# Kernel tuning notes

Hardware: AMD Instinct MI355X
Metric: run time of the kernel (lower is better)

## Reference

```python
import jax, jax.numpy as jnp
import numpy as np

L2 = (0.01, 0.01)
L1_RATIO = 0.5
EPS = 1e-16


def soft_thresholding(x, t):
    return jnp.sign(x) * jnp.maximum(jnp.abs(x) - t, 0.0)


def update_u(x, u, v, l1, l2, eps=EPS):
    # x: [B,M,N], u: [B,M,R], v: [B,N,R]
    a = jnp.einsum('bmn,bnr->bmr', x, v)      # x @ v            [B,M,R]
    b = jnp.einsum('bnr,bns->brs', v, v)      # v.mT @ v         [B,R,R]
    R = u.shape[-1]

    def step(u_new, r):
        # Gauss-Seidel update of column r using the freshest u_new (sequential dependency)
        br = jnp.take(b, r, axis=-1)                        # b[..., :, r]   [B,R]
        brr = jnp.take(br, r, axis=-1)                      # b[..., r, r]   [B]
        # term2 = u_new[..., indices] @ b[..., indices, r] computed as full matvec minus the r-th term
        term2 = jnp.einsum('bmk,bk->bm', u_new, br) - jnp.take(u_new, r, axis=-1) * brr[:, None]
        num = soft_thresholding(jnp.take(a, r, axis=-1) - term2, l1)   # [B,M]
        den = brr[:, None] + l2                                        # [B,1]
        ur = (num + eps) / (den + eps)
        return u_new.at[..., r].set(ur), None

    u_new, _ = jax.lax.scan(step, u, jnp.arange(R))
    return u_new


def setup_inputs() -> dict:
    key = jax.random.key(0)
    k1, k2, k3 = jax.random.split(key, 3)
    B, M, N, R = 8, 2048, 2048, 32
    x = jax.random.normal(k1, (B, M, N), dtype=jnp.float32)
    u = jax.random.normal(k2, (B, M, R), dtype=jnp.float32)
    v = jax.random.normal(k3, (B, N, R), dtype=jnp.float32)
    return {"x": x, "u": u, "v": v}


def reference(x, u, v):
    M, N = x.shape[-2], x.shape[-1]
    l1_u = L2[0] * L1_RATIO * N
    l2_u = L2[0] * (1.0 - L1_RATIO) * N
    l1_v = L2[1] * L1_RATIO * M
    l2_v = L2[1] * (1.0 - L1_RATIO) * M
    u = update_u(x, u, v, l1_u, l2_u)                              # factor 0
    v = update_u(jnp.swapaxes(x, -1, -2), v, u, l1_v, l2_v)        # factor 1 (update_v)
    return (u, v)
```

## Files before the change

kernel.cpp:

```cpp
#include <hip/hip_runtime.h>
#include <hip/hip_bf16.h>

#define NB 8
#define MD 2048
#define RD 32
#define KSPLIT 4
#define KSL (2048 / KSPLIT)
#define VT_STRIDE 520
#define XT_STRIDE 40
#define ASL ((size_t)NB * 2048 * RD)

typedef float floatx4 __attribute__((ext_vector_type(4)));
typedef short shortx8 __attribute__((ext_vector_type(8)));

static __device__ __forceinline__ short f2b(float f) {
    __hip_bfloat16 h = __float2bfloat16(f);
    return (short)*reinterpret_cast<unsigned short*>(&h);
}

static __device__ __forceinline__ void bmat_part(const float* __restrict__ w,
                                                 float* __restrict__ bp,
                                                 int bz, int t, char* smem) {
    int batch = bz >> 5;
    int slice = bz & 31;
    float* ws = (float*)smem;
    const float* wb = w + ((size_t)batch * 2048 + slice * 64) * RD;
#pragma unroll
    for (int i = 0; i < 8; ++i) {
        int idx = t + i * 256;
        ws[(idx >> 5) * 36 + (idx & 31)] = wb[(idx >> 5) * RD + (idx & 31)];
    }
    __syncthreads();
    int ii = t >> 3;
    int jq = (t & 7) * 4;
    float a0 = 0.f, a1 = 0.f, a2 = 0.f, a3 = 0.f;
    for (int n = 0; n < 64; ++n) {
        float wi = ws[n * 36 + ii];
        float4 wj = *(const float4*)&ws[n * 36 + jq];
        a0 = fmaf(wi, wj.x, a0);
        a1 = fmaf(wi, wj.y, a1);
        a2 = fmaf(wi, wj.z, a2);
        a3 = fmaf(wi, wj.w, a3);
    }
    float4 r = {a0, a1, a2, a3};
    *(float4*)(bp + (((size_t)batch * 32 + slice) * RD + ii) * RD + jq) = r;
}

__global__ __launch_bounds__(256, 4) void fused1_kernel(const float* __restrict__ x,
                                                        const float* __restrict__ v,
                                                        float* __restrict__ ap,
                                                        float* __restrict__ bp) {
    __shared__ __align__(16) char smem[32 * VT_STRIDE * 2];
    int bz = blockIdx.x;
    int t = threadIdx.x;
    if (bz < NB * 32) {
        bmat_part(v, bp, bz, t, smem);
        return;
    }
    bz -= NB * 32;
    short* wT = (short*)smem;
    int ks = bz & (KSPLIT - 1);
    int mblk = (bz >> 2) & 31;
    int batch = bz >> 7;
    int lane = t & 63;
    int wave = t >> 6;

    const float* wb = v + ((size_t)batch * 2048 + ks * KSL) * RD;
#pragma unroll
    for (int i = 0; i < 16; ++i) {
        int idx = t + i * 256;
        int k = idx >> 3;
        int rq = (idx & 7) * 4;
        float4 f = *(const float4*)(wb + (size_t)k * RD + rq);
        wT[(rq + 0) * VT_STRIDE + k] = f2b(f.x);
        wT[(rq + 1) * VT_STRIDE + k] = f2b(f.y);
        wT[(rq + 2) * VT_STRIDE + k] = f2b(f.z);
        wT[(rq + 3) * VT_STRIDE + k] = f2b(f.w);
    }
    __syncthreads();

    int kq = (lane >> 4) * 8;
    const float* xrow =
        x + ((size_t)batch * MD + mblk * 64 + wave * 16 + (lane & 15)) * 2048 + ks * KSL + kq;
    int r0 = (lane & 15) * VT_STRIDE + kq;
    int r1 = ((lane & 15) + 16) * VT_STRIDE + kq;

    floatx4 acc0 = {0.f, 0.f, 0.f, 0.f}, acc1 = {0.f, 0.f, 0.f, 0.f};
    float4 fa = *(const float4*)(xrow);
    float4 fb = *(const float4*)(xrow + 4);
    for (int s = 0; s < KSL / 32; ++s) {
        float4 na = {0, 0, 0, 0}, nb = {0, 0, 0, 0};
        if (s + 1 < KSL / 32) {
            na = *(const float4*)(xrow + (s + 1) * 32);
            nb = *(const float4*)(xrow + (s + 1) * 32 + 4);
        }
        shortx8 af = {f2b(fa.x), f2b(fa.y), f2b(fa.z), f2b(fa.w),
                      f2b(fb.x), f2b(fb.y), f2b(fb.z), f2b(fb.w)};
        shortx8 b0 = *(const shortx8*)&wT[r0 + s * 32];
        shortx8 b1 = *(const shortx8*)&wT[r1 + s * 32];
        acc0 = __builtin_amdgcn_mfma_f32_16x16x32_bf16(af, b0, acc0, 0, 0, 0);
        acc1 = __builtin_amdgcn_mfma_f32_16x16x32_bf16(af, b1, acc1, 0, 0, 0);
        fa = na;
        fb = nb;
    }
    float* ab = ap + ks * ASL +
                ((size_t)batch * 2048 + mblk * 64 + wave * 16 + (lane >> 4) * 4) * RD +
                (lane & 15);
#pragma unroll
    for (int i = 0; i < 4; ++i) {
        ab[i * RD] = acc0[i];
        ab[i * RD + 16] = acc1[i];
    }
}

__global__ __launch_bounds__(256, 4) void fused2_kernel(const float* __restrict__ x,
                                                        const float* __restrict__ u,
                                                        float* __restrict__ ap,
                                                        float* __restrict__ bp) {
    __shared__ __align__(16) short smem[32 * VT_STRIDE + 4 * 16 * XT_STRIDE];
    int bz = blockIdx.x;
    int t = threadIdx.x;
    if (bz < NB * 32) {
        bmat_part(u, bp, bz, t, (char*)smem);
        return;
    }
    bz -= NB * 32;
    short* uT = smem;
    short* xT = smem + 32 * VT_STRIDE;
    int ks = bz & (KSPLIT - 1);
    int nblk = (bz >> 2) & 31;
    int batch = bz >> 7;
    int lane = t & 63;
    int wave = t >> 6;

    const float* ub = u + ((size_t)batch * 2048 + ks * KSL) * RD;
#pragma unroll
    for (int i = 0; i < 16; ++i) {
        int idx = t + i * 256;
        int k = idx >> 3;
        int rq = (idx & 7) * 4;
        float4 f = *(const float4*)(ub + (size_t)k * RD + rq);
        uT[(rq + 0) * VT_STRIDE + k] = f2b(f.x);
        uT[(rq + 1) * VT_STRIDE + k] = f2b(f.y);
        uT[(rq + 2) * VT_STRIDE + k] = f2b(f.z);
        uT[(rq + 3) * VT_STRIDE + k] = f2b(f.w);
    }
    __syncthreads();

    short* xTw = &xT[wave * 16 * XT_STRIDE];
    int mloc = lane & 31;
    int ng = (lane >> 5) * 8;
    int n0w = nblk * 64 + wave * 16;
    const float* xp = x + ((size_t)batch * 2048 + ks * KSL + mloc) * 2048 + n0w + ng;

    int nl = lane & 15;
    int kq = (lane >> 4) * 8;
    int rA = nl * XT_STRIDE + kq;
    int rB0 = nl * VT_STRIDE + kq;
    int rB1 = (nl + 16) * VT_STRIDE + kq;

    floatx4 acc0 = {0.f, 0.f, 0.f, 0.f}, acc1 = {0.f, 0.f, 0.f, 0.f};
    float4 fa = *(const float4*)xp;
    float4 fb = *(const float4*)(xp + 4);
    for (int s = 0; s < KSL / 32; ++s) {
        xTw[(ng + 0) * XT_STRIDE + mloc] = f2b(fa.x);
        xTw[(ng + 1) * XT_STRIDE + mloc] = f2b(fa.y);
        xTw[(ng + 2) * XT_STRIDE + mloc] = f2b(fa.z);
        xTw[(ng + 3) * XT_STRIDE + mloc] = f2b(fa.w);
        xTw[(ng + 4) * XT_STRIDE + mloc] = f2b(fb.x);
        xTw[(ng + 5) * XT_STRIDE + mloc] = f2b(fb.y);
        xTw[(ng + 6) * XT_STRIDE + mloc] = f2b(fb.z);
        xTw[(ng + 7) * XT_STRIDE + mloc] = f2b(fb.w);
        float4 na = {0, 0, 0, 0}, nb = {0, 0, 0, 0};
        if (s + 1 < KSL / 32) {
            na = *(const float4*)(xp + (size_t)(s + 1) * 32 * 2048);
            nb = *(const float4*)(xp + (size_t)(s + 1) * 32 * 2048 + 4);
        }
        shortx8 af = *(const shortx8*)&xTw[rA];
        shortx8 b0 = *(const shortx8*)&uT[rB0 + s * 32];
        shortx8 b1 = *(const shortx8*)&uT[rB1 + s * 32];
        acc0 = __builtin_amdgcn_mfma_f32_16x16x32_bf16(af, b0, acc0, 0, 0, 0);
        acc1 = __builtin_amdgcn_mfma_f32_16x16x32_bf16(af, b1, acc1, 0, 0, 0);
        fa = na;
        fb = nb;
    }
    float* ab = ap + ks * ASL +
                ((size_t)batch * 2048 + n0w + (lane >> 4) * 4) * RD + (lane & 15);
#pragma unroll
    for (int i = 0; i < 4; ++i) {
        ab[i * RD] = acc0[i];
        ab[i * RD + 16] = acc1[i];
    }
}

__global__ __launch_bounds__(256) void gs_kernel(const float* __restrict__ uin,
                                                 const float* __restrict__ ap,
                                                 const float* __restrict__ bp,
                                                 float* __restrict__ uout,
                                                 float l1, float l2) {
    int blk = blockIdx.x;
    int batch = blk >> 3;
    int m = (blk & 7) * 256 + threadIdx.x;
    __shared__ float bs[RD][RD];
    {
        const float4* bpp = (const float4*)(bp + (size_t)batch * 32 * RD * RD) + threadIdx.x;
        float4 bacc = {0.f, 0.f, 0.f, 0.f};
#pragma unroll
        for (int s = 0; s < 32; ++s) {
            float4 f = bpp[s * 256];
            bacc.x += f.x;
            bacc.y += f.y;
            bacc.z += f.z;
            bacc.w += f.w;
        }
        ((float4*)&bs[0][0])[threadIdx.x] = bacc;
    }
    __syncthreads();
    float uv[RD], av[RD];
    const float* up = uin + ((size_t)batch * 2048 + m) * RD;
    const float* app = ap + ((size_t)batch * 2048 + m) * RD;
#pragma unroll
    for (int q = 0; q < 8; ++q) {
        *(float4*)&uv[q * 4] = *(const float4*)&up[q * 4];
        float4 s0 = *(const float4*)(app + q * 4);
        float4 s1 = *(const float4*)(app + ASL + q * 4);
        float4 s2 = *(const float4*)(app + 2 * ASL + q * 4);
        float4 s3 = *(const float4*)(app + 3 * ASL + q * 4);
        float4 r;
        r.x = (s0.x + s1.x) + (s2.x + s3.x);
        r.y = (s0.y + s1.y) + (s2.y + s3.y);
        r.z = (s0.z + s1.z) + (s2.z + s3.z);
        r.w = (s0.w + s1.w) + (s2.w + s3.w);
        *(float4*)&av[q * 4] = r;
    }
#pragma unroll
    for (int r = 0; r < RD; ++r) {
        float brr = bs[r][r];
        float4 t2v = {0.f, 0.f, 0.f, 0.f};
#pragma unroll
        for (int q = 0; q < 8; ++q) {
            float4 bq = *(const float4*)&bs[r][q * 4];
            t2v.x = fmaf(uv[q * 4 + 0], bq.x, t2v.x);
            t2v.y = fmaf(uv[q * 4 + 1], bq.y, t2v.y);
            t2v.z = fmaf(uv[q * 4 + 2], bq.z, t2v.z);
            t2v.w = fmaf(uv[q * 4 + 3], bq.w, t2v.w);
        }
        float t2 = ((t2v.x + t2v.y) + (t2v.z + t2v.w)) - uv[r] * brr;
        float num = av[r] - t2;
        float mag = fmaxf(fabsf(num) - l1, 0.f);
        num = copysignf(mag, num);
        uv[r] = (num + 1e-16f) / (brr + l2 + 1e-16f);
    }
    float* op = uout + ((size_t)batch * 2048 + m) * RD;
#pragma unroll
    for (int q = 0; q < 8; ++q) *(float4*)&op[q * 4] = *(float4*)&uv[q * 4];
}

extern "C" void kernel_launch(void* const* d_in, const int* in_sizes, int n_in,
                              void* d_out, int out_size, void* d_ws, size_t ws_size,
                              hipStream_t stream) {
    const float* x = (const float*)d_in[0];
    const float* u = (const float*)d_in[1];
    const float* v = (const float*)d_in[2];
    float* out_u = (float*)d_out;
    float* out_v = out_u + (size_t)NB * MD * RD;
    float* ap = (float*)d_ws;
    float* bp = ap + KSPLIT * ASL;
    const float l1u = 10.24f, l2u = 10.24f;
    const float l1v = 10.24f, l2v = 10.24f;
    const int GRID = NB * 32 + NB * 32 * KSPLIT;

    fused1_kernel<<<GRID, 256, 0, stream>>>(x, v, ap, bp);
    gs_kernel<<<NB * 8, 256, 0, stream>>>(u, ap, bp, out_u, l1u, l2u);

    fused2_kernel<<<GRID, 256, 0, stream>>>(x, out_u, ap, bp);
    gs_kernel<<<NB * 8, 256, 0, stream>>>(v, ap, bp, out_v, l1v, l2v);
}
```

Measured before the change: 253.7 us.

## Double K-split, interleave partial sums per row, and spread GS over more blocks

Result: no change. 257.3 us (+1.4%).

```diff
diff --git a/kernel.cpp b/kernel.cpp
--- a/kernel.cpp
+++ b/kernel.cpp
@@ -4,11 +4,11 @@
 #define NB 8
 #define MD 2048
 #define RD 32
-#define KSPLIT 4
+#define KSPLIT 8
 #define KSL (2048 / KSPLIT)
-#define VT_STRIDE 520
+#define VT_STRIDE 264
 #define XT_STRIDE 40
-#define ASL ((size_t)NB * 2048 * RD)
+#define GEMM_BLOCKS (NB * 32 * KSPLIT)
 
 typedef float floatx4 __attribute__((ext_vector_type(4)));
 typedef short shortx8 __attribute__((ext_vector_type(8)));
@@ -46,7 +46,7 @@
     *(float4*)(bp + (((size_t)batch * 32 + slice) * RD + ii) * RD + jq) = r;
 }
 
-__global__ __launch_bounds__(256, 4) void fused1_kernel(const float* __restrict__ x,
+__global__ __launch_bounds__(256, 8) void fused1_kernel(const float* __restrict__ x,
                                                         const float* __restrict__ v,
                                                         float* __restrict__ ap,
                                                         float* __restrict__ bp) {
@@ -60,14 +60,14 @@
     bz -= NB * 32;
     short* wT = (short*)smem;
     int ks = bz & (KSPLIT - 1);
-    int mblk = (bz >> 2) & 31;
-    int batch = bz >> 7;
+    int mblk = (bz >> 3) & 31;
+    int batch = bz >> 8;
     int lane = t & 63;
     int wave = t >> 6;
 
     const float* wb = v + ((size_t)batch * 2048 + ks * KSL) * RD;
 #pragma unroll
-    for (int i = 0; i < 16; ++i) {
+    for (int i = 0; i < 8; ++i) {
         int idx = t + i * 256;
         int k = idx >> 3;
         int rq = (idx & 7) * 4;
@@ -103,17 +103,17 @@
         fa = na;
         fb = nb;
     }
-    float* ab = ap + ks * ASL +
-                ((size_t)batch * 2048 + mblk * 64 + wave * 16 + (lane >> 4) * 4) * RD +
+    float* ab = ap +
+                (((size_t)batch * 2048 + mblk * 64 + wave * 16 + (lane >> 4) * 4) * KSPLIT + ks) * RD +
                 (lane & 15);
 #pragma unroll
     for (int i = 0; i < 4; ++i) {
-        ab[i * RD] = acc0[i];
-        ab[i * RD + 16] = acc1[i];
-    }
-}
-
-__global__ __launch_bounds__(256, 4) void fused2_kernel(const float* __restrict__ x,
+        ab[i * KSPLIT * RD] = acc0[i];
+        ab[i * KSPLIT * RD + 16] = acc1[i];
+    }
+}
+
+__global__ __launch_bounds__(256, 8) void fused2_kernel(const float* __restrict__ x,
                                                         const float* __restrict__ u,
                                                         float* __restrict__ ap,
                                                         float* __restrict__ bp) {
@@ -128,14 +128,14 @@
     short* uT = smem;
     short* xT = smem + 32 * VT_STRIDE;
     int ks = bz & (KSPLIT - 1);
-    int nblk = (bz >> 2) & 31;
-    int batch = bz >> 7;
+    int nblk = (bz >> 3) & 31;
+    int batch = bz >> 8;
     int lane = t & 63;
     int wave = t >> 6;
 
     const float* ub = u + ((size_t)batch * 2048 + ks * KSL) * RD;
 #pragma unroll
-    for (int i = 0; i < 16; ++i) {
+    for (int i = 0; i < 8; ++i) {
         int idx = t + i * 256;
         int k = idx >> 3;
         int rq = (idx & 7) * 4;
@@ -184,12 +184,13 @@
         fa = na;
         fb = nb;
     }
-    float* ab = ap + ks * ASL +
-                ((size_t)batch * 2048 + n0w + (lane >> 4) * 4) * RD + (lane & 15);
+    float* ab = ap +
+                (((size_t)batch * 2048 + n0w + (lane >> 4) * 4) * KSPLIT + ks) * RD +
+                (lane & 15);
 #pragma unroll
     for (int i = 0; i < 4; ++i) {
-        ab[i * RD] = acc0[i];
-        ab[i * RD + 16] = acc1[i];
+        ab[i * KSPLIT * RD] = acc0[i];
+        ab[i * KSPLIT * RD + 16] = acc1[i];
     }
 }
 
@@ -198,10 +199,9 @@
                                                  const float* __restrict__ bp,
                                                  float* __restrict__ uout,
                                                  float l1, float l2) {
-    int blk = blockIdx.x;
-    int batch = blk >> 3;
-    int m = (blk & 7) * 256 + threadIdx.x;
-    __shared__ float bs[RD][RD];
+    int bz = blockIdx.x;
+    int batch = bz >> 5;
+    __shared__ float bs[RD * RD];
     {
         const float4* bpp = (const float4*)(bp + (size_t)batch * 32 * RD * RD) + threadIdx.x;
         float4 bacc = {0.f, 0.f, 0.f, 0.f};
@@ -213,33 +213,36 @@
             bacc.z += f.z;
             bacc.w += f.w;
         }
-        ((float4*)&bs[0][0])[threadIdx.x] = bacc;
-    }
-    __syncthreads();
+        ((float4*)bs)[threadIdx.x] = bacc;
+    }
+    __syncthreads();
+    int t = threadIdx.x;
+    if (t >= 64) return;
+    int m = (bz & 31) * 64 + t;
     float uv[RD], av[RD];
     const float* up = uin + ((size_t)batch * 2048 + m) * RD;
-    const float* app = ap + ((size_t)batch * 2048 + m) * RD;
+    const float* app = ap + ((size_t)batch * 2048 + m) * (KSPLIT * RD);
 #pragma unroll
     for (int q = 0; q < 8; ++q) {
         *(float4*)&uv[q * 4] = *(const float4*)&up[q * 4];
-        float4 s0 = *(const float4*)(app + q * 4);
-        float4 s1 = *(const float4*)(app + ASL + q * 4);
-        float4 s2 = *(const float4*)(app + 2 * ASL + q * 4);
-        float4 s3 = *(const float4*)(app + 3 * ASL + q * 4);
-        float4 r;
-        r.x = (s0.x + s1.x) + (s2.x + s3.x);
-        r.y = (s0.y + s1.y) + (s2.y + s3.y);
-        r.z = (s0.z + s1.z) + (s2.z + s3.z);
-        r.w = (s0.w + s1.w) + (s2.w + s3.w);
+        float4 r = {0.f, 0.f, 0.f, 0.f};
+#pragma unroll
+        for (int s = 0; s < KSPLIT; ++s) {
+            float4 f = *(const float4*)(app + s * RD + q * 4);
+            r.x += f.x;
+            r.y += f.y;
+            r.z += f.z;
+            r.w += f.w;
+        }
         *(float4*)&av[q * 4] = r;
     }
 #pragma unroll
     for (int r = 0; r < RD; ++r) {
-        float brr = bs[r][r];
+        float brr = bs[r * RD + r];
         float4 t2v = {0.f, 0.f, 0.f, 0.f};
 #pragma unroll
         for (int q = 0; q < 8; ++q) {
-            float4 bq = *(const float4*)&bs[r][q * 4];
+            float4 bq = *(const float4*)&bs[r * RD + q * 4];
             t2v.x = fmaf(uv[q * 4 + 0], bq.x, t2v.x);
             t2v.y = fmaf(uv[q * 4 + 1], bq.y, t2v.y);
             t2v.z = fmaf(uv[q * 4 + 2], bq.z, t2v.z);
@@ -265,14 +268,14 @@
     float* out_u = (float*)d_out;
     float* out_v = out_u + (size_t)NB * MD * RD;
     float* ap = (float*)d_ws;
-    float* bp = ap + KSPLIT * ASL;
+    float* bp = ap + (size_t)NB * 2048 * KSPLIT * RD;
     const float l1u = 10.24f, l2u = 10.24f;
     const float l1v = 10.24f, l2v = 10.24f;
-    const int GRID = NB * 32 + NB * 32 * KSPLIT;
+    const int GRID = NB * 32 + GEMM_BLOCKS;
 
     fused1_kernel<<<GRID, 256, 0, stream>>>(x, v, ap, bp);
-    gs_kernel<<<NB * 8, 256, 0, stream>>>(u, ap, bp, out_u, l1u, l2u);
+    gs_kernel<<<NB * 32, 256, 0, stream>>>(u, ap, bp, out_u, l1u, l2u);
 
     fused2_kernel<<<GRID, 256, 0, stream>>>(x, out_u, ap, bp);
-    gs_kernel<<<NB * 8, 256, 0, stream>>>(v, ap, bp, out_v, l1v, l2v);
-}
+    gs_kernel<<<NB * 32, 256, 0, stream>>>(v, ap, bp, out_v, l1v, l2v);
+}
```
